# Optimization experiments

Measured on AMD Instinct MI355X. Metric: run time of the kernel, lower is better.

The kernel has to match this reference:

```python
import jax, jax.numpy as jnp
import numpy as np

B, S, D_MODEL, N_HEADS = 2, 2048, 2048, 16
D_K = D_MODEL // N_HEADS
MAX_SEQ_LEN = 4096


def _rope_tables(seq_len, d_k):
    # matches RotaryPositionalEmbedding buffers
    inv_freq = 1.0 / (10000.0 ** (jnp.arange(0, d_k, 2, dtype=jnp.float32) / d_k))
    pos = jnp.arange(seq_len, dtype=jnp.float32)
    freqs = pos[:, None] * inv_freq[None, :]  # [S, d_k/2]
    return jnp.cos(freqs), jnp.sin(freqs)


def _apply_rope(x, cos, sin):
    # x: [B, H, S, d_k]; cos/sin: [S, d_k/2] -> broadcast [1,1,S,d_k/2]
    cos = cos[None, None, :, :]
    sin = sin[None, None, :, :]
    x_even = x[..., ::2]
    x_odd = x[..., 1::2]
    r_even = x_even * cos - x_odd * sin
    r_odd = x_even * sin + x_odd * cos
    return jnp.stack([r_even, r_odd], axis=-1).reshape(x.shape)


def setup_inputs() -> dict:
    key = jax.random.key(0)
    ks = jax.random.split(key, 5)
    scale = 1.0 / np.sqrt(D_MODEL)
    return {
        "x": jax.random.normal(ks[0], (B, S, D_MODEL), jnp.float32),
        "wq_w": jax.random.normal(ks[1], (D_MODEL, D_MODEL), jnp.float32) * scale,
        "wq_b": jnp.zeros((D_MODEL,), jnp.float32),
        "wk_w": jax.random.normal(ks[2], (D_MODEL, D_MODEL), jnp.float32) * scale,
        "wk_b": jnp.zeros((D_MODEL,), jnp.float32),
        "wv_w": jax.random.normal(ks[3], (D_MODEL, D_MODEL), jnp.float32) * scale,
        "wv_b": jnp.zeros((D_MODEL,), jnp.float32),
        "wo_w": jax.random.normal(ks[4], (D_MODEL, D_MODEL), jnp.float32) * scale,
        "wo_b": jnp.zeros((D_MODEL,), jnp.float32),
    }


def reference(x, wq_w, wq_b, wk_w, wk_b, wv_w, wv_b, wo_w, wo_b):
    b, s, _ = x.shape
    # QKV projections (torch Linear: x @ W.T + b), split heads -> [B, H, S, d_k]
    def proj(w, bias):
        y = jnp.einsum('bsd,ed->bse', x, w) + bias
        return y.reshape(b, s, N_HEADS, D_K).transpose(0, 2, 1, 3)

    q = proj(wq_w, wq_b)
    k = proj(wk_w, wk_b)
    v = proj(wv_w, wv_b)

    cos, sin = _rope_tables(s, D_K)
    q = _apply_rope(q, cos, sin)
    k = _apply_rope(k, cos, sin)

    # causal SDPA
    scale = 1.0 / np.sqrt(D_K).astype(np.float32)
    scores = jnp.einsum('bhqd,bhkd->bhqk', q, k) * scale
    causal = jnp.tril(jnp.ones((s, s), dtype=bool))
    scores = jnp.where(causal[None, None, :, :], scores, jnp.float32(-jnp.inf))
    attn = jax.nn.softmax(scores, axis=-1)
    out = jnp.einsum('bhqk,bhkd->bhqd', attn, v)

    out = out.transpose(0, 2, 1, 3).reshape(b, s, D_MODEL)
    return jnp.einsum('bsd,ed->bse', out, wo_w) + wo_b
```

## Files before the change

kernel.cpp:

```cpp
#include <hip/hip_runtime.h>


#define DMODEL 2048
#define SEQ    2048
#define NHEAD  16
#define DKH    128
#define NBATCH 2
#define MTOK   (NBATCH*SEQ)

typedef float  f32x4  __attribute__((ext_vector_type(4)));
typedef __bf16 bf16x8 __attribute__((ext_vector_type(8)));
typedef unsigned short      u16;
typedef unsigned short      u16x4 __attribute__((ext_vector_type(4)));

#if __has_builtin(__builtin_amdgcn_exp2f)
#define EXP2F __builtin_amdgcn_exp2f
#else
#define EXP2F exp2f
#endif

__device__ __forceinline__ float b2f(u16 u) {
    union { unsigned i; float f; } x; x.i = ((unsigned)u) << 16; return x.f;
}
__device__ __forceinline__ u16 f2bf(float f) {
    union { float f; unsigned i; } x; x.f = f;
    unsigned r = x.i + 0x7fffu + ((x.i >> 16) & 1u);
    return (u16)(r >> 16);
}

__device__ __forceinline__ void load_lds16(const void* g, void* l) {
    __builtin_amdgcn_global_load_lds(
        (const __attribute__((address_space(1))) void*)g,
        (__attribute__((address_space(3))) void*)l, 16, 0, 0);
}

struct CastArgs {
    const float* src[5];
    u16*         dst[5];
    int          n4[5];
};
__global__ void cast_all_kernel(CastArgs a) {
    int j = blockIdx.y;
    int i = blockIdx.x * blockDim.x + threadIdx.x;
    if (i >= a.n4[j]) return;
    float4 f = ((const float4*)a.src[j])[i];
    uint2 o;
    o.x = (unsigned)f2bf(f.x) | ((unsigned)f2bf(f.y) << 16);
    o.y = (unsigned)f2bf(f.z) | ((unsigned)f2bf(f.w) << 16);
    ((uint2*)a.dst[j])[i] = o;
}

__global__ __launch_bounds__(256) void gemm_qkv(
    const u16* __restrict__ A, const u16* __restrict__ W,
    const float* __restrict__ qb, const float* __restrict__ kb,
    const float* __restrict__ vb,
    u16* __restrict__ QB, u16* __restrict__ KB, u16* __restrict__ VT)
{
    __shared__ u16 As[128 * 64];
    __shared__ u16 Bs[128 * 64];
    const int tid  = threadIdx.x;
    const int lane = tid & 63;
    const int w    = tid >> 6;
    const int wm   = w >> 1, wn = w & 1;
    const int quad = lane >> 4, l16 = lane & 15;
    const int row0 = blockIdx.y * 128;
    const int col0 = blockIdx.x * 128;
    const int K    = DMODEL;

    f32x4 acc[4][4] = {};

    for (int kt = 0; kt < K / 64; ++kt) {
        const int k0 = kt * 64;
#pragma unroll
        for (int i = 0; i < 4; ++i) {
            int cb = (i * 4 + w) * 64;
            int p  = cb + lane;
            int r  = p >> 3;
            int cl = (p & 7) ^ (r & 7);
            load_lds16(A + (size_t)(row0 + r) * K + k0 + cl * 8, (void*)(As + cb * 8));
            load_lds16(W + (size_t)(col0 + r) * K + k0 + cl * 8, (void*)(Bs + cb * 8));
        }
        __syncthreads();
#pragma unroll
        for (int ks = 0; ks < 2; ++ks) {
            bf16x8 af[4], bfr[4];
#pragma unroll
            for (int mi = 0; mi < 4; ++mi) {
                int r  = wm * 64 + mi * 16 + l16;
                int pc = (ks * 4 + quad) ^ (r & 7);
                af[mi] = *(const bf16x8*)(As + (r * 8 + pc) * 8);
            }
#pragma unroll
            for (int ni = 0; ni < 4; ++ni) {
                int r  = wn * 64 + ni * 16 + l16;
                int pc = (ks * 4 + quad) ^ (r & 7);
                bfr[ni] = *(const bf16x8*)(Bs + (r * 8 + pc) * 8);
            }
#pragma unroll
            for (int mi = 0; mi < 4; ++mi)
#pragma unroll
                for (int ni = 0; ni < 4; ++ni)
                    acc[mi][ni] = __builtin_amdgcn_mfma_f32_16x16x32_bf16(
                        af[mi], bfr[ni], acc[mi][ni], 0, 0, 0);
        }
        __syncthreads();
    }

    const int sect = col0 >> 11;
    if (sect == 2) {
#pragma unroll
        for (int mi = 0; mi < 4; ++mi) {
#pragma unroll
            for (int ni = 0; ni < 4; ++ni) {
                int colv = (col0 & 2047) + wn * 64 + ni * 16 + l16;
                float bv = vb[colv];
                int rowb = row0 + wm * 64 + mi * 16 + quad * 4;
                int bb = rowb >> 11, s = rowb & 2047;
                u16x4 pk;
#pragma unroll
                for (int r = 0; r < 4; ++r) pk[r] = f2bf(acc[mi][ni][r] + bv);
                *(u16x4*)(VT + (size_t)(bb * 2048 + colv) * 2048 + s) = pk;
            }
        }
    } else {
        const float* bias = sect ? kb : qb;
        u16* dst          = sect ? KB : QB;
#pragma unroll
        for (int mi = 0; mi < 4; ++mi) {
#pragma unroll
            for (int ni = 0; ni < 4; ++ni) {
                int col = (col0 & 2047) + wn * 64 + ni * 16 + l16;
                float bv = bias[col];
#pragma unroll
                for (int r = 0; r < 4; ++r) {
                    int row = row0 + wm * 64 + mi * 16 + quad * 4 + r;
                    dst[(size_t)row * 2048 + col] = f2bf(acc[mi][ni][r] + bv);
                }
            }
        }
    }
}

__global__ void rope_kernel(u16* __restrict__ Q, u16* __restrict__ Kt) {
    int idx = blockIdx.x * blockDim.x + threadIdx.x;
    u16* P      = blockIdx.y ? Kt : Q;
    float scale = blockIdx.y ? 1.0f : 0.12751743558f;
    int i   = idx & 63;
    int tok = idx >> 10;
    int s   = tok & (SEQ - 1);
    unsigned pr = *(const unsigned*)(P + 2 * (size_t)idx);
    float e = b2f((u16)(pr & 0xffff)), o = b2f((u16)(pr >> 16));
    float inv_freq = exp2f(-13.287712379549449f * (float)i * (1.0f / 64.0f));
    float ang = (float)s * inv_freq;
    float c, sn;
    sincosf(ang, &sn, &c);
    float re = (e * c - o * sn) * scale;
    float ro = (e * sn + o * c) * scale;
    *(unsigned*)(P + 2 * (size_t)idx) = (unsigned)f2bf(re) | ((unsigned)f2bf(ro) << 16);
}

__global__ __launch_bounds__(512, 4) void attn_kernel(
    const u16* __restrict__ Q, const u16* __restrict__ Kg,
    const u16* __restrict__ VTg, u16* __restrict__ Out)
{
    const int p  = blockIdx.x;
    const int bh = blockIdx.y;
    const int b  = bh >> 4, h = bh & 15;

    const int tid  = threadIdx.x;
    const int lane = tid & 63;
    const int w    = tid >> 6;
    const int half = w >> 2;
    const int wsub = w & 3;
    const int quad = lane >> 4, l16 = lane & 15;

    const int q_hi  = 31 - p;
    const int my_qt = half ? q_hi : p;
    const int q0    = my_qt * 64;

    __shared__ u16 Ks[64 * 128];
    __shared__ u16 Vt[128 * 64];
    __shared__ u16 Ps[8][16 * 72];

    bf16x8 qf[4];
    const u16* qrow = Q + (size_t)(b * SEQ + q0 + wsub * 16 + l16) * DMODEL + h * DKH;
#pragma unroll
    for (int ks = 0; ks < 4; ++ks) qf[ks] = *(const bf16x8*)(qrow + ks * 32 + quad * 8);

    f32x4 o[8] = {};
    float l_r[4] = { 0.f, 0.f, 0.f, 0.f };

    for (int kt = 0; kt <= q_hi; ++kt) {
        const int k0 = kt * 64;
#pragma unroll
        for (int i = 0; i < 2; ++i) {
            int cb = (i * 8 + w) * 64;
            int pc = cb + lane;
            int r  = pc >> 4;
            int cl = (pc & 15) ^ (r & 15);
            load_lds16(Kg + (size_t)(b * SEQ + k0 + r) * DMODEL + h * DKH + cl * 8,
                       (void*)(Ks + cb * 8));
        }
#pragma unroll
        for (int i = 0; i < 2; ++i) {
            int cb = (i * 8 + w) * 64;
            int pc = cb + lane;
            int r  = pc >> 3;
            int cl = (pc & 7) ^ (r & 7);
            load_lds16(VTg + (size_t)(b * 2048 + h * DKH + r) * SEQ + k0 + cl * 8,
                       (void*)(Vt + cb * 8));
        }
        __syncthreads();

        if (kt <= my_qt) {
            f32x4 sc[4] = {};
#pragma unroll
            for (int ks = 0; ks < 4; ++ks) {
#pragma unroll
                for (int nt = 0; nt < 4; ++nt) {
                    int r  = nt * 16 + l16;
                    int pc = (ks * 4 + quad) ^ (r & 15);
                    bf16x8 kf = *(const bf16x8*)(Ks + (r * 16 + pc) * 8);
                    sc[nt] = __builtin_amdgcn_mfma_f32_16x16x32_bf16(qf[ks], kf, sc[nt], 0, 0, 0);
                }
            }
            if (kt == my_qt) {
#pragma unroll
                for (int nt = 0; nt < 4; ++nt)
#pragma unroll
                    for (int r = 0; r < 4; ++r) {
                        int col = k0 + nt * 16 + l16;
                        int row = q0 + wsub * 16 + quad * 4 + r;
                        if (col > row) sc[nt][r] = -1e30f;
                    }
            }
#pragma unroll
            for (int nt = 0; nt < 4; ++nt)
#pragma unroll
                for (int r = 0; r < 4; ++r) {
                    float pv = EXP2F(sc[nt][r] - 32.0f);
                    l_r[r] += pv;
                    Ps[w][(quad * 4 + r) * 72 + nt * 16 + l16] = f2bf(pv);
                }
#pragma unroll
            for (int ks = 0; ks < 2; ++ks) {
                bf16x8 pf = *(const bf16x8*)(&Ps[w][l16 * 72 + ks * 32 + quad * 8]);
#pragma unroll
                for (int nt = 0; nt < 8; ++nt) {
                    int r  = nt * 16 + l16;
                    int pc = (ks * 4 + quad) ^ (r & 7);
                    bf16x8 vf = *(const bf16x8*)(Vt + r * 64 + pc * 8);
                    o[nt] = __builtin_amdgcn_mfma_f32_16x16x32_bf16(pf, vf, o[nt], 0, 0, 0);
                }
            }
        }
        __syncthreads();
    }

#pragma unroll
    for (int r = 0; r < 4; ++r) {
#pragma unroll
        for (int off = 1; off < 16; off <<= 1) l_r[r] += __shfl_xor(l_r[r], off);
        float inv = 1.0f / l_r[r];
        int row = q0 + wsub * 16 + quad * 4 + r;
#pragma unroll
        for (int nt = 0; nt < 8; ++nt)
            Out[(size_t)(b * SEQ + row) * DMODEL + h * DKH + nt * 16 + l16] = f2bf(o[nt][r] * inv);
    }
}

__global__ __launch_bounds__(256) void gemm_o(
    const u16* __restrict__ A, const u16* __restrict__ W,
    const float* __restrict__ bias, float* __restrict__ Cout,
    int M, int N, int K)
{
    __shared__ u16 As[128 * 64];
    __shared__ u16 Bs[128 * 64];
    const int tid  = threadIdx.x;
    const int lane = tid & 63;
    const int w    = tid >> 6;
    const int wm   = w >> 1, wn = w & 1;
    const int quad = lane >> 4, l16 = lane & 15;
    const int row0 = blockIdx.y * 128;
    const int col0 = blockIdx.x * 128;

    f32x4 acc[4][4] = {};

    for (int kt = 0; kt < K / 64; ++kt) {
        const int k0 = kt * 64;
#pragma unroll
        for (int i = 0; i < 4; ++i) {
            int cb = (i * 4 + w) * 64;
            int p  = cb + lane;
            int r  = p >> 3;
            int cl = (p & 7) ^ (r & 7);
            load_lds16(A + (size_t)(row0 + r) * K + k0 + cl * 8, (void*)(As + cb * 8));
            load_lds16(W + (size_t)(col0 + r) * K + k0 + cl * 8, (void*)(Bs + cb * 8));
        }
        __syncthreads();
#pragma unroll
        for (int ks = 0; ks < 2; ++ks) {
            bf16x8 af[4], bfr[4];
#pragma unroll
            for (int mi = 0; mi < 4; ++mi) {
                int r  = wm * 64 + mi * 16 + l16;
                int pc = (ks * 4 + quad) ^ (r & 7);
                af[mi] = *(const bf16x8*)(As + (r * 8 + pc) * 8);
            }
#pragma unroll
            for (int ni = 0; ni < 4; ++ni) {
                int r  = wn * 64 + ni * 16 + l16;
                int pc = (ks * 4 + quad) ^ (r & 7);
                bfr[ni] = *(const bf16x8*)(Bs + (r * 8 + pc) * 8);
            }
#pragma unroll
            for (int mi = 0; mi < 4; ++mi)
#pragma unroll
                for (int ni = 0; ni < 4; ++ni)
                    acc[mi][ni] = __builtin_amdgcn_mfma_f32_16x16x32_bf16(
                        af[mi], bfr[ni], acc[mi][ni], 0, 0, 0);
        }
        __syncthreads();
    }
#pragma unroll
    for (int mi = 0; mi < 4; ++mi) {
#pragma unroll
        for (int ni = 0; ni < 4; ++ni) {
            int col = col0 + wn * 64 + ni * 16 + l16;
            float bv = bias[col];
#pragma unroll
            for (int r = 0; r < 4; ++r) {
                int row = row0 + wm * 64 + mi * 16 + quad * 4 + r;
                Cout[(size_t)row * N + col] = acc[mi][ni][r] + bv;
            }
        }
    }
}

extern "C" void kernel_launch(void* const* d_in, const int* in_sizes, int n_in,
                              void* d_out, int out_size, void* d_ws, size_t ws_size,
                              hipStream_t stream)
{
    const float* x    = (const float*)d_in[0];
    const float* wq_w = (const float*)d_in[1];
    const float* wq_b = (const float*)d_in[2];
    const float* wk_w = (const float*)d_in[3];
    const float* wk_b = (const float*)d_in[4];
    const float* wv_w = (const float*)d_in[5];
    const float* wv_b = (const float*)d_in[6];
    const float* wo_w = (const float*)d_in[7];
    const float* wo_b = (const float*)d_in[8];
    float* out = (float*)d_out;

    char* ws = (char*)d_ws;
    u16* XB   = (u16*)(ws);
    u16* WQKV = (u16*)(ws + (16u << 20));
    u16* WOB  = (u16*)(ws + (40u << 20));
    u16* QB   = (u16*)(ws + (48u << 20));
    u16* KB   = (u16*)(ws + (64u << 20));
    u16* VTB  = (u16*)(ws + (80u << 20));

    CastArgs ca;
    ca.src[0] = x;    ca.dst[0] = XB;                         ca.n4[0] = (MTOK * DMODEL) / 4;
    ca.src[1] = wq_w; ca.dst[1] = WQKV;                       ca.n4[1] = (DMODEL * DMODEL) / 4;
    ca.src[2] = wk_w; ca.dst[2] = WQKV + DMODEL * DMODEL;     ca.n4[2] = (DMODEL * DMODEL) / 4;
    ca.src[3] = wv_w; ca.dst[3] = WQKV + 2 * DMODEL * DMODEL; ca.n4[3] = (DMODEL * DMODEL) / 4;
    ca.src[4] = wo_w; ca.dst[4] = WOB;                        ca.n4[4] = (DMODEL * DMODEL) / 4;
    cast_all_kernel<<<dim3(8192, 5), 256, 0, stream>>>(ca);

    gemm_qkv<<<dim3(48, 32), 256, 0, stream>>>(XB, WQKV, wq_b, wk_b, wv_b, QB, KB, VTB);

    rope_kernel<<<dim3((MTOK * NHEAD * 64) / 256, 2), 256, 0, stream>>>(QB, KB);

    attn_kernel<<<dim3(16, NBATCH * NHEAD), 512, 0, stream>>>(QB, KB, VTB, XB);

    gemm_o<<<dim3(16, 32), 256, 0, stream>>>(XB, WOB, wo_b, out, MTOK, DMODEL, DMODEL);
}
```

Before: 383.8 us.

## Restructure attention blocks to pair adjacent query tiles with 32-row warps

```diff
diff --git a/kernel.cpp b/kernel.cpp
--- a/kernel.cpp
+++ b/kernel.cpp
@@ -18,6 +18,13 @@
 #else
 #define EXP2F exp2f
 #endif
+#if __has_builtin(__builtin_amdgcn_sinf)
+#define SINR __builtin_amdgcn_sinf
+#define COSR __builtin_amdgcn_cosf
+#else
+__device__ __forceinline__ float SINR(float r){ return sinf(r * 6.283185307179586f); }
+__device__ __forceinline__ float COSR(float r){ return cosf(r * 6.283185307179586f); }
+#endif
 
 __device__ __forceinline__ float b2f(u16 u) {
     union { unsigned i; float f; } x; x.i = ((unsigned)u) << 16; return x.f;
@@ -26,6 +33,10 @@
     union { float f; unsigned i; } x; x.f = f;
     unsigned r = x.i + 0x7fffu + ((x.i >> 16) & 1u);
     return (u16)(r >> 16);
+}
+__device__ __forceinline__ u16 f2bf_fast(float f) {
+    union { float f; unsigned i; } x; x.f = f;
+    return (u16)((x.i + 0x8000u) >> 16);
 }
 
 __device__ __forceinline__ void load_lds16(const void* g, void* l) {
@@ -150,51 +161,54 @@
     int s   = tok & (SEQ - 1);
     unsigned pr = *(const unsigned*)(P + 2 * (size_t)idx);
     float e = b2f((u16)(pr & 0xffff)), o = b2f((u16)(pr >> 16));
-    float inv_freq = exp2f(-13.287712379549449f * (float)i * (1.0f / 64.0f));
-    float ang = (float)s * inv_freq;
-    float c, sn;
-    sincosf(ang, &sn, &c);
+    float invf_rev = exp2f(-0.2076205059304601f * (float)i) * 0.15915494309189535f;
+    float rev = (float)s * invf_rev;
+    rev -= floorf(rev);
+    float c = COSR(rev), sn = SINR(rev);
     float re = (e * c - o * sn) * scale;
     float ro = (e * sn + o * c) * scale;
     *(unsigned*)(P + 2 * (size_t)idx) = (unsigned)f2bf(re) | ((unsigned)f2bf(ro) << 16);
 }
 
-__global__ __launch_bounds__(512, 4) void attn_kernel(
+__global__ __launch_bounds__(256, 3) void attn_kernel(
     const u16* __restrict__ Q, const u16* __restrict__ Kg,
     const u16* __restrict__ VTg, u16* __restrict__ Out)
 {
-    const int p  = blockIdx.x;
-    const int bh = blockIdx.y;
+    const int ip = 15 - (blockIdx.x >> 5);
+    const int bh = blockIdx.x & 31;
     const int b  = bh >> 4, h = bh & 15;
 
     const int tid  = threadIdx.x;
     const int lane = tid & 63;
-    const int w    = tid >> 6;
-    const int half = w >> 2;
-    const int wsub = w & 3;
+    const int wv   = tid >> 6;
+    const int g    = wv >> 1;
+    const int hs   = wv & 1;
     const int quad = lane >> 4, l16 = lane & 15;
 
-    const int q_hi  = 31 - p;
-    const int my_qt = half ? q_hi : p;
-    const int q0    = my_qt * 64;
+    const int my_qt = 2 * ip + g;
+    const int kmax  = 2 * ip + 1;
+    const int q0    = my_qt * 64 + hs * 32;
 
     __shared__ u16 Ks[64 * 128];
     __shared__ u16 Vt[128 * 64];
-    __shared__ u16 Ps[8][16 * 72];
-
-    bf16x8 qf[4];
-    const u16* qrow = Q + (size_t)(b * SEQ + q0 + wsub * 16 + l16) * DMODEL + h * DKH;
-#pragma unroll
-    for (int ks = 0; ks < 4; ++ks) qf[ks] = *(const bf16x8*)(qrow + ks * 32 + quad * 8);
-
-    f32x4 o[8] = {};
-    float l_r[4] = { 0.f, 0.f, 0.f, 0.f };
-
-    for (int kt = 0; kt <= q_hi; ++kt) {
+    __shared__ u16 Ps[4][32 * 72];
+
+    bf16x8 qf[2][4];
+#pragma unroll
+    for (int mi = 0; mi < 2; ++mi) {
+        const u16* qrow = Q + (size_t)(b * SEQ + q0 + mi * 16 + l16) * DMODEL + h * DKH;
+#pragma unroll
+        for (int ks = 0; ks < 4; ++ks) qf[mi][ks] = *(const bf16x8*)(qrow + ks * 32 + quad * 8);
+    }
+
+    f32x4 o[2][8] = {};
+    float l_r[2][4] = {};
+
+    for (int kt = 0; kt <= kmax; ++kt) {
         const int k0 = kt * 64;
 #pragma unroll
-        for (int i = 0; i < 2; ++i) {
-            int cb = (i * 8 + w) * 64;
+        for (int i = 0; i < 4; ++i) {
+            int cb = (i * 4 + wv) * 64;
             int pc = cb + lane;
             int r  = pc >> 4;
             int cl = (pc & 15) ^ (r & 15);
@@ -202,8 +216,8 @@
                        (void*)(Ks + cb * 8));
         }
 #pragma unroll
-        for (int i = 0; i < 2; ++i) {
-            int cb = (i * 8 + w) * 64;
+        for (int i = 0; i < 4; ++i) {
+            int cb = (i * 4 + wv) * 64;
             int pc = cb + lane;
             int r  = pc >> 3;
             int cl = (pc & 7) ^ (r & 7);
@@ -213,7 +227,7 @@
         __syncthreads();
 
         if (kt <= my_qt) {
-            f32x4 sc[4] = {};
+            f32x4 sc[2][4] = {};
 #pragma unroll
             for (int ks = 0; ks < 4; ++ks) {
 #pragma unroll
@@ -221,36 +235,43 @@
                     int r  = nt * 16 + l16;
                     int pc = (ks * 4 + quad) ^ (r & 15);
                     bf16x8 kf = *(const bf16x8*)(Ks + (r * 16 + pc) * 8);
-                    sc[nt] = __builtin_amdgcn_mfma_f32_16x16x32_bf16(qf[ks], kf, sc[nt], 0, 0, 0);
+                    sc[0][nt] = __builtin_amdgcn_mfma_f32_16x16x32_bf16(qf[0][ks], kf, sc[0][nt], 0, 0, 0);
+                    sc[1][nt] = __builtin_amdgcn_mfma_f32_16x16x32_bf16(qf[1][ks], kf, sc[1][nt], 0, 0, 0);
                 }
             }
             if (kt == my_qt) {
 #pragma unroll
+                for (int mi = 0; mi < 2; ++mi)
+#pragma unroll
+                    for (int nt = 0; nt < 4; ++nt)
+#pragma unroll
+                        for (int r = 0; r < 4; ++r) {
+                            int col = k0 + nt * 16 + l16;
+                            int row = q0 + mi * 16 + quad * 4 + r;
+                            if (col > row) sc[mi][nt][r] = -1e30f;
+                        }
+            }
+#pragma unroll
+            for (int mi = 0; mi < 2; ++mi)
+#pragma unroll
                 for (int nt = 0; nt < 4; ++nt)
 #pragma unroll
                     for (int r = 0; r < 4; ++r) {
-                        int col = k0 + nt * 16 + l16;
-                        int row = q0 + wsub * 16 + quad * 4 + r;
-                        if (col > row) sc[nt][r] = -1e30f;
+                        float pv = EXP2F(sc[mi][nt][r] - 32.0f);
+                        l_r[mi][r] += pv;
+                        Ps[wv][(mi * 16 + quad * 4 + r) * 72 + nt * 16 + l16] = f2bf_fast(pv);
                     }
-            }
-#pragma unroll
-            for (int nt = 0; nt < 4; ++nt)
-#pragma unroll
-                for (int r = 0; r < 4; ++r) {
-                    float pv = EXP2F(sc[nt][r] - 32.0f);
-                    l_r[r] += pv;
-                    Ps[w][(quad * 4 + r) * 72 + nt * 16 + l16] = f2bf(pv);
-                }
 #pragma unroll
             for (int ks = 0; ks < 2; ++ks) {
-                bf16x8 pf = *(const bf16x8*)(&Ps[w][l16 * 72 + ks * 32 + quad * 8]);
+                bf16x8 pf0 = *(const bf16x8*)(&Ps[wv][(l16) * 72 + ks * 32 + quad * 8]);
+                bf16x8 pf1 = *(const bf16x8*)(&Ps[wv][(16 + l16) * 72 + ks * 32 + quad * 8]);
 #pragma unroll
                 for (int nt = 0; nt < 8; ++nt) {
                     int r  = nt * 16 + l16;
                     int pc = (ks * 4 + quad) ^ (r & 7);
                     bf16x8 vf = *(const bf16x8*)(Vt + r * 64 + pc * 8);
-                    o[nt] = __builtin_amdgcn_mfma_f32_16x16x32_bf16(pf, vf, o[nt], 0, 0, 0);
+                    o[0][nt] = __builtin_amdgcn_mfma_f32_16x16x32_bf16(pf0, vf, o[0][nt], 0, 0, 0);
+                    o[1][nt] = __builtin_amdgcn_mfma_f32_16x16x32_bf16(pf1, vf, o[1][nt], 0, 0, 0);
                 }
             }
         }
@@ -258,15 +279,19 @@
     }
 
 #pragma unroll
-    for (int r = 0; r < 4; ++r) {
-#pragma unroll
-        for (int off = 1; off < 16; off <<= 1) l_r[r] += __shfl_xor(l_r[r], off);
-        float inv = 1.0f / l_r[r];
-        int row = q0 + wsub * 16 + quad * 4 + r;
-#pragma unroll
-        for (int nt = 0; nt < 8; ++nt)
-            Out[(size_t)(b * SEQ + row) * DMODEL + h * DKH + nt * 16 + l16] = f2bf(o[nt][r] * inv);
-    }
+    for (int mi = 0; mi < 2; ++mi)
+#pragma unroll
+        for (int r = 0; r < 4; ++r) {
+            float lv = l_r[mi][r];
+#pragma unroll
+            for (int off = 1; off < 16; off <<= 1) lv += __shfl_xor(lv, off);
+            float inv = 1.0f / lv;
+            int row = q0 + mi * 16 + quad * 4 + r;
+#pragma unroll
+            for (int nt = 0; nt < 8; ++nt)
+                Out[(size_t)(b * SEQ + row) * DMODEL + h * DKH + nt * 16 + l16] =
+                    f2bf(o[mi][nt][r] * inv);
+        }
 }
 
 __global__ __launch_bounds__(256) void gemm_o(
@@ -372,7 +397,7 @@
 
     rope_kernel<<<dim3((MTOK * NHEAD * 64) / 256, 2), 256, 0, stream>>>(QB, KB);
 
-    attn_kernel<<<dim3(16, NBATCH * NHEAD), 512, 0, stream>>>(QB, KB, VTB, XB);
+    attn_kernel<<<512, 256, 0, stream>>>(QB, KB, VTB, XB);
 
     gemm_o<<<dim3(16, 32), 256, 0, stream>>>(XB, WOB, wo_b, out, MTOK, DMODEL, DMODEL);
 }
```

After: 433.5 us. +12.9%, slower.
